# Optimization experiments

Hardware: AMD Instinct MI355X
Metric: run time of the kernel (lower is better)

Reference implementation:

```python
import jax, jax.numpy as jnp
import numpy as np

D_MODEL = 2048
NUM_HEADS = 16
NUM_KV_HEADS = 4
HEAD_DIM = D_MODEL // NUM_HEADS  # 128
B, T = 2, 2048


def setup_inputs() -> dict:
    key = jax.random.key(0)
    ks = jax.random.split(key, 9)
    d_kv = NUM_KV_HEADS * HEAD_DIM
    s = 1.0 / np.sqrt(D_MODEL)
    return {
        "x": jax.random.normal(ks[0], (B, T, D_MODEL), dtype=jnp.float32),
        "Wq": jax.random.normal(ks[1], (D_MODEL, D_MODEL), dtype=jnp.float32) * s,
        "bq": jnp.zeros((D_MODEL,), dtype=jnp.float32),
        "Wk": jax.random.normal(ks[2], (D_MODEL, d_kv), dtype=jnp.float32) * s,
        "bk": jnp.zeros((d_kv,), dtype=jnp.float32),
        "Wv": jax.random.normal(ks[3], (D_MODEL, d_kv), dtype=jnp.float32) * s,
        "bv": jnp.zeros((d_kv,), dtype=jnp.float32),
        "Wo": jax.random.normal(ks[4], (D_MODEL, D_MODEL), dtype=jnp.float32) * s,
        "bo": jnp.zeros((D_MODEL,), dtype=jnp.float32),
    }


def reference(x, Wq, bq, Wk, bk, Wv, bv, Wo, bo):
    b, t, _ = x.shape
    # projections
    q = x @ Wq + bq                      # [B,T,D]
    k = x @ Wk + bk                      # [B,T,KVH*Dh]
    v = x @ Wv + bv
    q = q.reshape(b, t, NUM_HEADS, HEAD_DIM)      # [B,T,H,Dh]
    k = k.reshape(b, t, NUM_KV_HEADS, HEAD_DIM)   # [B,T,KVH,Dh]
    v = v.reshape(b, t, NUM_KV_HEADS, HEAD_DIM)
    repeat = NUM_HEADS // NUM_KV_HEADS
    k = jnp.repeat(k, repeat, axis=2)              # [B,T,H,Dh]
    v = jnp.repeat(v, repeat, axis=2)
    scores = jnp.einsum('bthd,bshd->bhts', q, k) / jnp.sqrt(
        jnp.asarray(HEAD_DIM, dtype=x.dtype))
    mask = jnp.tril(jnp.ones((t, t), dtype=x.dtype))
    # faithful to source: multiplicative mask plus large negative on masked
    scores = scores * mask - 1e10 * (1.0 - mask)
    probs = jax.nn.softmax(scores, axis=-1)        # [B,H,T,S]
    out = jnp.einsum('bhts,bshd->bthd', probs, v)  # [B,T,H,Dh]
    out = out.reshape(b, t, NUM_HEADS * HEAD_DIM)  # merge heads
    return out @ Wo + bo                           # [B,T,D]
```

## Files before the change

kernel.cpp:

```cpp
#include <hip/hip_runtime.h>

typedef __attribute__((ext_vector_type(8))) __bf16 bf16x8;
typedef __attribute__((ext_vector_type(4))) float f32x4;
typedef __attribute__((ext_vector_type(4))) short short4v;

#define MFMA16(a,b,c)  __builtin_amdgcn_mfma_f32_16x16x32_bf16((a),(b),(c),0,0,0)
#define MFMA16K(a,b,c) __builtin_amdgcn_mfma_f32_16x16x16bf16_1k((a),(b),(c),0,0,0)

__device__ __forceinline__ short f2bf(float f){
  union { float f; unsigned u; } x; x.f = f;
  return (short)((x.u + 0x7fffu + ((x.u >> 16) & 1u)) >> 16);
}
__device__ __forceinline__ unsigned bits(float f){
  union { float f; unsigned u; } x; x.f = f; return x.u;
}

__device__ __forceinline__ void gld16(void* lds, const void* g){
  __builtin_amdgcn_global_load_lds(
      (const __attribute__((address_space(1))) unsigned*)g,
      (__attribute__((address_space(3))) unsigned*)lds, 16, 0, 0);
}

template<int N>
__device__ __forceinline__ void s_wait_vmcnt(){
  if constexpr (N==8)      asm volatile("s_waitcnt vmcnt(8)" ::: "memory");
  else if constexpr (N==6) asm volatile("s_waitcnt vmcnt(6)" ::: "memory");
  else if constexpr (N==4) asm volatile("s_waitcnt vmcnt(4)" ::: "memory");
  else if constexpr (N==2) asm volatile("s_waitcnt vmcnt(2)" ::: "memory");
  else                     asm volatile("s_waitcnt vmcnt(0)" ::: "memory");
}


__global__ __launch_bounds__(256) void k_cvt8(const float* __restrict__ x,
                                              short* __restrict__ xb){
  long i = (long)blockIdx.x * 256 + threadIdx.x;
  const float4* xv = (const float4*)x;
  float4 a = xv[2*i], c = xv[2*i+1];
  short s[8] = {f2bf(a.x),f2bf(a.y),f2bf(a.z),f2bf(a.w),
                f2bf(c.x),f2bf(c.y),f2bf(c.z),f2bf(c.w)};
  *(uint4*)&xb[8*i] = *(uint4*)s;
}

__global__ void k_wt(const float* __restrict__ W, short* __restrict__ Wt, int N){
  __shared__ float tile[32][33];
  int tx = threadIdx.x, ty = threadIdx.y;
  int k0 = blockIdx.y*32, n0 = blockIdx.x*32;
  for (int j=0;j<32;j+=8)
    tile[ty+j][tx] = W[(size_t)(k0+ty+j)*N + n0 + tx];
  __syncthreads();
  for (int j=0;j<32;j+=8)
    Wt[(size_t)(n0+ty+j)*2048 + k0 + tx] = f2bf(tile[tx][ty+j]);
}

__global__ void k_bias(const float* __restrict__ bq, const float* __restrict__ bk,
                       const float* __restrict__ bv, float* __restrict__ outb){
  int i = blockIdx.x*256 + threadIdx.x;
  float v = (i < 2048) ? bq[i] : (i < 2560 ? bk[i-2048] : bv[i-2560]);
  outb[i] = v;
}

__global__ void k_vt(const short* __restrict__ qkv, short* __restrict__ Vt){
  __shared__ short tile[32][33];
  int tx = threadIdx.x, ty = threadIdx.y;
  int t0 = blockIdx.x*32, c0 = blockIdx.y*32;
  for (int j=0;j<32;j+=8)
    tile[ty+j][tx] = qkv[(size_t)(t0+ty+j)*3072 + 2560 + c0 + tx];
  __syncthreads();
  int b = t0 >> 11, t_in_b = t0 & 2047;
  for (int j=0;j<32;j+=8){
    int col = c0 + ty + j;
    int kvh = col >> 7, d = col & 127;
    Vt[((size_t)((b*4 + kvh)*128 + d))*2048 + t_in_b + tx] = tile[tx][ty+j];
  }
}

template<int BCH, int OUT_BF16>
__global__ __launch_bounds__(512, 2) void gemmR(const short* __restrict__ A,
    const short* __restrict__ Bt, const float* __restrict__ bias,
    void* __restrict__ Cv, int N, int K){
  constexpr int ASZ  = 8192;
  constexpr int BUFS = ASZ*(1+BCH);
  __shared__ short SM[2*BUFS];
  const int tid = threadIdx.x;
  const int w = tid >> 6, lane = tid & 63, l15 = lane & 15, quad = lane >> 4;
  const int wr = w >> 2, wc = w & 3;
  const int m0 = blockIdx.y * 128, n0 = blockIdx.x * (BCH*128);
  const int ln8 = lane >> 3;
  const int g8 = (((lane & 7) ^ ln8) << 3);
  const short* aB = A  + (size_t)(m0 + w*16 + ln8) * K + g8;
  const short* bB = Bt + (size_t)(n0 + w*16 + ln8) * K + g8;
  const int aRB = (wr*64 + l15)*64;
  const int bRB = (wc*32 + l15)*64;
  const int phys0 = ((quad     ^ (l15 & 7)) << 3);
  const int phys1 = (((quad+4) ^ (l15 & 7)) << 3);
  f32x4 acc[BCH][4][2] = {};
  bf16x8 aF[4][2], bF[2][2];
  const int nt = K >> 6;

#define STG_A(bufi, T) do{ \
    short* d_ = &SM[(bufi)*BUFS + w*1024]; \
    const short* s_ = aB + (size_t)(T)*64; \
    gld16(d_, s_); gld16(d_+512, s_ + (size_t)8*K); }while(0)
#define STG_B(bufi, ch, T) do{ \
    short* d_ = &SM[(bufi)*BUFS + ASZ + (ch)*ASZ + w*1024]; \
    const short* s_ = bB + (size_t)((ch)*128)*K + (size_t)(T)*64; \
    gld16(d_, s_); gld16(d_+512, s_ + (size_t)8*K); }while(0)
#define RD_A(bufi) do{ const short* p_ = &SM[(bufi)*BUFS + aRB]; \
    _Pragma("unroll") for(int m_=0;m_<4;m_++){ \
      aF[m_][0] = *(const bf16x8*)&p_[m_*1024 + phys0]; \
      aF[m_][1] = *(const bf16x8*)&p_[m_*1024 + phys1]; } }while(0)
#define RD_B(bufi, ch) do{ const short* p_ = &SM[(bufi)*BUFS + ASZ + (ch)*ASZ + bRB]; \
    _Pragma("unroll") for(int n_=0;n_<2;n_++){ \
      bF[n_][0] = *(const bf16x8*)&p_[n_*1024 + phys0]; \
      bF[n_][1] = *(const bf16x8*)&p_[n_*1024 + phys1]; } }while(0)
#define MM(ch) do{ __builtin_amdgcn_s_setprio(1); \
    _Pragma("unroll") for(int m_=0;m_<4;m_++) \
    _Pragma("unroll") for(int n_=0;n_<2;n_++){ \
      acc[ch][m_][n_] = MFMA16(aF[m_][0], bF[n_][0], acc[ch][m_][n_]); \
      acc[ch][m_][n_] = MFMA16(aF[m_][1], bF[n_][1], acc[ch][m_][n_]); } \
    __builtin_amdgcn_s_setprio(0); }while(0)
#define PH(W) do{ s_wait_vmcnt<W>(); \
    __builtin_amdgcn_s_barrier(); \
    __builtin_amdgcn_sched_barrier(0); }while(0)
#define GROUP3(T, ST1, ST2, W0, W1, W2) do{ \
    const int c_=(T)&1, n_c=c_^1; \
    PH(W0); if (ST1) STG_B(n_c,1,(T)+1); RD_A(c_); RD_B(c_,0); MM(0); \
    PH(W1); if (ST1) STG_B(n_c,2,(T)+1); RD_B(c_,1); MM(1); \
    PH(W2); if (ST2){ STG_A(c_,(T)+2); STG_B(c_,0,(T)+2); } RD_B(c_,2); MM(2); \
  }while(0)
#define GROUP2(T, ST1, ST2, W0, W1) do{ \
    const int c_=(T)&1, n_c=c_^1; \
    PH(W0); if (ST1) STG_B(n_c,1,(T)+1); RD_A(c_); RD_B(c_,0); MM(0); \
    PH(W1); if (ST2){ STG_A(c_,(T)+2); STG_B(c_,0,(T)+2); } RD_B(c_,1); MM(1); \
  }while(0)

  if constexpr (BCH == 3){
    STG_A(0,0); STG_B(0,0,0); STG_B(0,1,0); STG_B(0,2,0);
    STG_A(1,1); STG_B(1,0,1);
    for (int T = 0; T < nt-2; ++T) GROUP3(T, true, true, 8,8,8);
    GROUP3(nt-2, true,  false, 8,8,8);
    GROUP3(nt-1, false, false, 4,2,0);
  } else {
    STG_A(0,0); STG_B(0,0,0); STG_B(0,1,0);
    STG_A(1,1); STG_B(1,0,1);
    for (int T = 0; T < nt-2; ++T) GROUP2(T, true, true, 6,6);
    GROUP2(nt-2, true,  false, 6,6);
    GROUP2(nt-1, false, false, 2,0);
  }

#undef GROUP2
#undef GROUP3
#undef PH
#undef MM
#undef RD_B
#undef RD_A
#undef STG_B
#undef STG_A

  float bv[BCH][2];
#pragma unroll
  for (int ch=0; ch<BCH; ch++)
#pragma unroll
    for (int n=0; n<2; n++)
      bv[ch][n] = bias[n0 + ch*128 + wc*32 + n*16 + l15];
#pragma unroll
  for (int ch=0; ch<BCH; ch++)
#pragma unroll
  for (int m=0; m<4; m++){
    int row = m0 + wr*64 + m*16 + quad*4;
#pragma unroll
    for (int n=0; n<2; n++){
      int col = n0 + ch*128 + wc*32 + n*16 + l15;
#pragma unroll
      for (int r=0; r<4; r++){
        float v = acc[ch][m][n][r] + bv[ch][n];
        if (OUT_BF16) ((short*)Cv)[(size_t)(row+r)*N + col] = f2bf(v);
        else          ((float*)Cv)[(size_t)(row+r)*N + col] = v;
      }
    }
  }
}

__global__ __launch_bounds__(256) void k_attn(const short* __restrict__ qkv,
                                              const short* __restrict__ Vt,
                                              short* __restrict__ attn){
  constexpr float COEF = 0.12752365f;
  __shared__ short SM[16384];
  const int tid = threadIdx.x, w = tid >> 6, lane = tid & 63;
  const int l15 = lane & 15, quad = lane >> 4;
  const int p = blockIdx.x, h = blockIdx.y, b = blockIdx.z, kvh = h >> 2;
  const int qi = ((h >> 3) & 1) ? p : 31 - p;

  const short* kb[2];
  const short* vb[2];
#pragma unroll
  for (int j=0;j<2;j++){
    int rK = w*8 + j*4 + (lane >> 4);
    int cK = (lane & 15) ^ (rK & 15);
    kb[j] = qkv + (size_t)(b*2048 + rK)*3072 + 2048 + kvh*128 + cK*8;
    int dV = w*32 + j*16 + (lane >> 2);
    int cV = (lane & 3) ^ (dV & 3) ^ ((dV >> 2) & 3);
    vb[j] = Vt + ((size_t)((b*4 + kvh)*128 + dV))*2048 + cV*8;
  }
  short* K0 = &SM[w*1024];
  short* V0 = &SM[4096 + w*1024];

  int buf = 0;
#pragma unroll
  for (int j=0;j<2;j++){
    gld16(K0 + j*512, kb[j]);
    gld16(V0 + j*512, vb[j]);
  }

  const int qw = qi*64 + w*16;
  bf16x8 qf[4];
  {
    const short* qbase = qkv + ((size_t)(b*2048 + qw + l15))*3072 + h*128 + quad*8;
#pragma unroll
    for (int d4=0;d4<4;d4++)
      qf[d4] = *(const bf16x8*)(qbase + d4*32);
  }
  f32x4 accO[8] = {};
  float lsum = 0.f;
  const int nst = 2*qi + 2;

  for (int st = 0; st < nst; st++){
    __syncthreads();
    const int cur = buf;
    const int nb = buf ^ 1;
    if (st + 1 < nst){
      int nxt = (st + 1) * 32;
      short* Kd = &SM[nb*8192 + w*1024];
      short* Vd = &SM[nb*8192 + 4096 + w*1024];
      const size_t ko = (size_t)nxt * 3072;
#pragma unroll
      for (int j=0;j<2;j++){
        gld16(Kd + j*512, kb[j] + ko);
        gld16(Vd + j*512, vb[j] + nxt);
      }
    }
    const int s0 = st * 32;
    if (s0 <= qw + 15){
      const short* Kb = &SM[cur*8192];
      const short* Vb = &SM[cur*8192 + 4096];
      bf16x8 kf[2][4];
#pragma unroll
      for (int ss=0;ss<2;ss++)
#pragma unroll
        for (int d4=0;d4<4;d4++){
          int slot = (ss*16 + l15)*16 + ((d4*4 + quad) ^ l15);
          kf[ss][d4] = *(const bf16x8*)&Kb[slot*8];
        }
      f32x4 sa[2] = {};
      __builtin_amdgcn_s_setprio(1);
#pragma unroll
      for (int d4=0;d4<4;d4++){
        sa[0] = MFMA16(kf[0][d4], qf[d4], sa[0]);
        sa[1] = MFMA16(kf[1][d4], qf[d4], sa[1]);
      }
      __builtin_amdgcn_s_setprio(0);
      short4v pf[2];
      const bool mneed = (s0 + 31 > qw);
      const int qgl = qw + l15;
#pragma unroll
      for (int sub=0;sub<2;sub++){
        float pr[4];
#pragma unroll
        for (int r=0;r<4;r++){
          float e = __builtin_amdgcn_exp2f(sa[sub][r] * COEF);
          int sg = s0 + sub*16 + quad*4 + r;
          if (mneed && (sg > qgl)) e = 0.f;
          pr[r] = e;
        }
        lsum += (pr[0]+pr[1]) + (pr[2]+pr[3]);
        union { unsigned u[2]; short4v s; } pk;
        pk.u[0] = __builtin_amdgcn_perm(bits(pr[1]), bits(pr[0]), 0x07060302u);
        pk.u[1] = __builtin_amdgcn_perm(bits(pr[3]), bits(pr[2]), 0x07060302u);
        pf[sub] = pk.s;
      }
      __builtin_amdgcn_s_setprio(1);
#pragma unroll
      for (int sub=0;sub<2;sub++)
#pragma unroll
        for (int dt=0;dt<8;dt++){
          int slot = (dt*16 + l15)*4 +
                     ((sub*2 + (quad>>1)) ^ (l15 & 3) ^ ((l15 >> 2) & 3));
          short4v vf = *(const short4v*)&Vb[slot*8 + (quad&1)*4];
          accO[dt] = MFMA16K(vf, pf[sub], accO[dt]);
        }
      __builtin_amdgcn_s_setprio(0);
    }
    buf = nb;
  }
  {
    float s = lsum;
    s += __shfl_xor(s, 16);
    s += __shfl_xor(s, 32);
    float inv = 1.0f / s;
    short* obase = attn + ((size_t)(b*2048 + qw + l15))*2048 + h*128 + quad*4;
#pragma unroll
    for (int dt=0;dt<8;dt++){
      float o0 = accO[dt][0]*inv, o1 = accO[dt][1]*inv;
      float o2 = accO[dt][2]*inv, o3 = accO[dt][3]*inv;
      union { unsigned u[2]; short4v s; } ok;
      ok.u[0] = __builtin_amdgcn_perm(bits(o1), bits(o0), 0x07060302u);
      ok.u[1] = __builtin_amdgcn_perm(bits(o3), bits(o2), 0x07060302u);
      *(short4v*)(obase + dt*16) = ok.s;
    }
  }
}

extern "C" void kernel_launch(void* const* d_in, const int* in_sizes, int n_in,
                              void* d_out, int out_size, void* d_ws, size_t ws_size,
                              hipStream_t stream){
  const float* x  = (const float*)d_in[0];
  const float* Wq = (const float*)d_in[1];
  const float* bq = (const float*)d_in[2];
  const float* Wk = (const float*)d_in[3];
  const float* bk = (const float*)d_in[4];
  const float* Wv = (const float*)d_in[5];
  const float* bv = (const float*)d_in[6];
  const float* Wo = (const float*)d_in[7];
  const float* bo = (const float*)d_in[8];
  float* out = (float*)d_out;
  char* ws = (char*)d_ws;

  short* xb    = (short*)(ws + 0);
  short* WtQKV = (short*)(ws + (size_t)16*1024*1024);
  short* WoT   = (short*)(ws + (size_t)28*1024*1024);
  float* biasQ = (float*)(ws + (size_t)36*1024*1024);
  short* qkv   = (short*)(ws + (size_t)37*1024*1024);
  short* Vt    = (short*)(ws + (size_t)61*1024*1024);
  short* attn  = (short*)(ws + 0);

  k_cvt8<<<4096, 256, 0, stream>>>(x, xb);
  k_wt<<<dim3(64,64), dim3(32,8), 0, stream>>>(Wq, WtQKV, 2048);
  k_wt<<<dim3(16,64), dim3(32,8), 0, stream>>>(Wk, WtQKV + (size_t)2048*2048, 512);
  k_wt<<<dim3(16,64), dim3(32,8), 0, stream>>>(Wv, WtQKV + (size_t)2560*2048, 512);
  k_wt<<<dim3(64,64), dim3(32,8), 0, stream>>>(Wo, WoT, 2048);
  k_bias<<<12, 256, 0, stream>>>(bq, bk, bv, biasQ);
  gemmR<3,1><<<dim3(8,32), 512, 0, stream>>>(xb, WtQKV, biasQ, qkv, 3072, 2048);
  k_vt<<<dim3(128,16), dim3(32,8), 0, stream>>>(qkv, Vt);
  k_attn<<<dim3(32,16,2), 256, 0, stream>>>(qkv, Vt, attn);
  gemmR<2,0><<<dim3(8,32), 512, 0, stream>>>(attn, WoT, bo, out, 2048, 2048);
}
```

Measured before the change: 316.6 us.

## Fuse weight-transpose launches, write V transpose in QKV epilogue, reorder attention blocks

Merges the four weight transpose/convert launches and the bias-concatenation launch into a single kernel that picks its source matrix from the block index. Removes the separate V-transpose kernel by having the QKV GEMM epilogue also scatter V columns into the transposed Vt buffer. Remaps attention blocks so the longest causal query tiles are dispatched first across all heads and batches. This trades launch overhead and an extra pass over V for strided 2-byte scatter stores in the GEMM epilogue, and the bias path is now rewritten redundantly by every y-block.

```diff
diff --git a/kernel.cpp b/kernel.cpp
--- a/kernel.cpp
+++ b/kernel.cpp
@@ -41,10 +41,27 @@
   *(uint4*)&xb[8*i] = *(uint4*)s;
 }
 
-__global__ void k_wt(const float* __restrict__ W, short* __restrict__ Wt, int N){
+__global__ void k_wtall(const float* __restrict__ Wq, const float* __restrict__ Wk,
+                        const float* __restrict__ Wv, const float* __restrict__ Wo,
+                        const float* __restrict__ bq, const float* __restrict__ bk,
+                        const float* __restrict__ bv,
+                        short* __restrict__ WtQKV, short* __restrict__ WoT,
+                        float* __restrict__ biasQ){
   __shared__ float tile[32][33];
   int tx = threadIdx.x, ty = threadIdx.y;
-  int k0 = blockIdx.y*32, n0 = blockIdx.x*32;
+  int bx = blockIdx.x;
+  if (bx >= 160){
+    int i = (bx - 160)*256 + ty*32 + tx;
+    float v = (i < 2048) ? bq[i] : (i < 2560 ? bk[i-2048] : bv[i-2560]);
+    biasQ[i] = v;
+    return;
+  }
+  const float* W; short* Wt; int N, nb0;
+  if (bx < 64)      { W = Wq; Wt = WtQKV;                      N = 2048; nb0 = bx; }
+  else if (bx < 80) { W = Wk; Wt = WtQKV + (size_t)2048*2048;  N = 512;  nb0 = bx-64; }
+  else if (bx < 96) { W = Wv; Wt = WtQKV + (size_t)2560*2048;  N = 512;  nb0 = bx-80; }
+  else              { W = Wo; Wt = WoT;                        N = 2048; nb0 = bx-96; }
+  int k0 = blockIdx.y*32, n0 = nb0*32;
   for (int j=0;j<32;j+=8)
     tile[ty+j][tx] = W[(size_t)(k0+ty+j)*N + n0 + tx];
   __syncthreads();
@@ -52,32 +69,10 @@
     Wt[(size_t)(n0+ty+j)*2048 + k0 + tx] = f2bf(tile[tx][ty+j]);
 }
 
-__global__ void k_bias(const float* __restrict__ bq, const float* __restrict__ bk,
-                       const float* __restrict__ bv, float* __restrict__ outb){
-  int i = blockIdx.x*256 + threadIdx.x;
-  float v = (i < 2048) ? bq[i] : (i < 2560 ? bk[i-2048] : bv[i-2560]);
-  outb[i] = v;
-}
-
-__global__ void k_vt(const short* __restrict__ qkv, short* __restrict__ Vt){
-  __shared__ short tile[32][33];
-  int tx = threadIdx.x, ty = threadIdx.y;
-  int t0 = blockIdx.x*32, c0 = blockIdx.y*32;
-  for (int j=0;j<32;j+=8)
-    tile[ty+j][tx] = qkv[(size_t)(t0+ty+j)*3072 + 2560 + c0 + tx];
-  __syncthreads();
-  int b = t0 >> 11, t_in_b = t0 & 2047;
-  for (int j=0;j<32;j+=8){
-    int col = c0 + ty + j;
-    int kvh = col >> 7, d = col & 127;
-    Vt[((size_t)((b*4 + kvh)*128 + d))*2048 + t_in_b + tx] = tile[tx][ty+j];
-  }
-}
-
-template<int BCH, int OUT_BF16>
+template<int BCH, int OUT_BF16, int WVT>
 __global__ __launch_bounds__(512, 2) void gemmR(const short* __restrict__ A,
     const short* __restrict__ Bt, const float* __restrict__ bias,
-    void* __restrict__ Cv, int N, int K){
+    void* __restrict__ Cv, short* __restrict__ Vt, int N, int K){
   constexpr int ASZ  = 8192;
   constexpr int BUFS = ASZ*(1+BCH);
   __shared__ short SM[2*BUFS];
@@ -174,8 +169,17 @@
 #pragma unroll
       for (int r=0; r<4; r++){
         float v = acc[ch][m][n][r] + bv[ch][n];
-        if (OUT_BF16) ((short*)Cv)[(size_t)(row+r)*N + col] = f2bf(v);
-        else          ((float*)Cv)[(size_t)(row+r)*N + col] = v;
+        if (OUT_BF16){
+          short sv = f2bf(v);
+          ((short*)Cv)[(size_t)(row+r)*N + col] = sv;
+          if (WVT && col >= 2560){
+            int c2 = col - 2560;
+            int rr = row + r;
+            Vt[((size_t)((rr>>11)*4 + (c2>>7))*128 + (c2&127))*2048 + (rr&2047)] = sv;
+          }
+        } else {
+          ((float*)Cv)[(size_t)(row+r)*N + col] = v;
+        }
       }
     }
   }
@@ -188,8 +192,10 @@
   __shared__ short SM[16384];
   const int tid = threadIdx.x, w = tid >> 6, lane = tid & 63;
   const int l15 = lane & 15, quad = lane >> 4;
-  const int p = blockIdx.x, h = blockIdx.y, b = blockIdx.z, kvh = h >> 2;
-  const int qi = ((h >> 3) & 1) ? p : 31 - p;
+  const int lin = (int)blockIdx.x + 32*(int)blockIdx.y + 512*(int)blockIdx.z;
+  const int qi  = 31 - (lin >> 5);
+  const int idx = lin & 31;
+  const int h = idx & 15, b = idx >> 4, kvh = h >> 2;
 
   const short* kb[2];
   const short* vb[2];
@@ -334,13 +340,9 @@
   short* attn  = (short*)(ws + 0);
 
   k_cvt8<<<4096, 256, 0, stream>>>(x, xb);
-  k_wt<<<dim3(64,64), dim3(32,8), 0, stream>>>(Wq, WtQKV, 2048);
-  k_wt<<<dim3(16,64), dim3(32,8), 0, stream>>>(Wk, WtQKV + (size_t)2048*2048, 512);
-  k_wt<<<dim3(16,64), dim3(32,8), 0, stream>>>(Wv, WtQKV + (size_t)2560*2048, 512);
-  k_wt<<<dim3(64,64), dim3(32,8), 0, stream>>>(Wo, WoT, 2048);
-  k_bias<<<12, 256, 0, stream>>>(bq, bk, bv, biasQ);
-  gemmR<3,1><<<dim3(8,32), 512, 0, stream>>>(xb, WtQKV, biasQ, qkv, 3072, 2048);
-  k_vt<<<dim3(128,16), dim3(32,8), 0, stream>>>(qkv, Vt);
+  k_wtall<<<dim3(172,64), dim3(32,8), 0, stream>>>(Wq, Wk, Wv, Wo, bq, bk, bv,
+                                                   WtQKV, WoT, biasQ);
+  gemmR<3,1,1><<<dim3(8,32), 512, 0, stream>>>(xb, WtQKV, biasQ, qkv, Vt, 3072, 2048);
   k_attn<<<dim3(32,16,2), 256, 0, stream>>>(qkv, Vt, attn);
-  gemmR<2,0><<<dim3(8,32), 512, 0, stream>>>(attn, WoT, bo, out, 2048, 2048);
-}
+  gemmR<2,0,0><<<dim3(8,32), 512, 0, stream>>>(attn, WoT, bo, out, nullptr, 2048, 2048);
+}
```

New measurement: 293.6 us. 7.3% less time.
